# Kernel optimization log

Hardware: AMD Instinct MI355X
Metric: run time of the kernel (lower is better)

Reference implementation:

```python
import jax, jax.numpy as jnp
import numpy as np

WIDTH = 256
HEAD = 16
SCALE = 2
G = WIDTH // HEAD          # 16 groups
NH = G * SCALE             # 32 kernelized heads
EPS = 1e-5
N_NODES = 20000
B_GRAPHS = 1024


def setup_inputs() -> dict:
    key = jax.random.key(0)
    ks = jax.random.split(key, 10)
    x = jax.random.normal(ks[0], (N_NODES, WIDTH), jnp.float32)
    x_res = jax.random.normal(ks[1], (B_GRAPHS, NH, HEAD, HEAD), jnp.float32)
    batch = jnp.sort(jax.random.randint(ks[2], (N_NODES,), 0, B_GRAPHS)).astype(jnp.int64)
    w_pre = jax.random.normal(ks[3], (WIDTH, WIDTH), jnp.float32) * 0.02
    b_pre = jnp.zeros((WIDTH,), jnp.float32)
    # grouped 1x1 convs: [groups, width_scale, head_out, head_in]
    wq = jax.random.normal(ks[4], (G, SCALE, HEAD, HEAD), jnp.float32) * 0.02
    wk = jax.random.normal(ks[5], (G, SCALE, HEAD, HEAD), jnp.float32) * 0.02
    wv = jax.random.normal(ks[6], (G, SCALE, HEAD, HEAD), jnp.float32) * 0.02
    w_post = jax.random.normal(ks[7], (WIDTH, WIDTH * SCALE), jnp.float32) * 0.02
    b_post = jnp.zeros((WIDTH,), jnp.float32)
    log_scale = jnp.full((WIDTH,), np.log(0.01), jnp.float32)
    return {"x": x, "x_res": x_res, "batch": batch, "batch_size": B_GRAPHS,
            "w_pre": w_pre, "b_pre": b_pre, "wq": wq, "wk": wk, "wv": wv,
            "w_post": w_post, "b_post": b_post, "log_scale": log_scale}


def reference(x, x_res, batch, batch_size, w_pre, b_pre, wq, wk, wv, w_post, b_post, log_scale):
    n = x.shape[0]
    # pre: 1x1 conv (= linear) + GroupNorm(affine=False); L=1 so normalize over
    # each group's width_head channels.
    y = x @ w_pre.T + b_pre                       # [N, width]
    yg = y.reshape(n, G, HEAD)                    # [N, G, Hd]
    mu = yg.mean(-1, keepdims=True)
    var = yg.var(-1, keepdims=True)               # biased, as in GroupNorm
    yn = (yg - mu) / jnp.sqrt(var + EPS)          # [N, G, Hd]

    inv_sqrt_h = 1.0 / np.sqrt(HEAD)
    # grouped convs -> kernelized q,k (exp) and v
    xq = jnp.exp(jnp.einsum('ngi,gsoi->ngso', yn, wq) * inv_sqrt_h).reshape(n, NH, HEAD)
    xk = jnp.exp(jnp.einsum('ngi,gsoi->ngso', yn, wk) * inv_sqrt_h).reshape(n, NH, HEAD)
    xv = jnp.einsum('ngi,gsoi->ngso', yn, wv).reshape(n, NH, HEAD)

    # outer product k (x) v then scatter-sum over graphs  [B, NH, Hd, Hd]
    kv = jnp.einsum('bnh,bnv->bnhv', xk, xv)
    kv_sum = jax.ops.segment_sum(kv, batch, num_segments=batch_size) + x_res
    x_res_out = kv_sum

    # per-graph key sum, gathered back to nodes
    k_sum = jax.ops.segment_sum(xk, batch, num_segments=batch_size)[batch]  # [N, NH, Hd]
    denom = jnp.einsum('bnh,bnh->bn', xq, k_sum)                            # [N, NH]
    qn = xq / denom[:, :, None]

    out = jnp.einsum('bnh,bnhv->bnv', qn, kv_sum[batch]).reshape(n, WIDTH * SCALE)
    out = jnp.exp(log_scale) * (out @ w_post.T + b_post)                    # [N, width]
    return (out, x_res_out)
```

## Files before the change

kernel.cpp:

```cpp
#include <hip/hip_runtime.h>
#include <stdint.h>

typedef unsigned int u32;
typedef unsigned short u16;
typedef __attribute__((ext_vector_type(8))) short v8s;
typedef __attribute__((ext_vector_type(4))) float v4f;

#define GN_EPS 1e-5f

__device__ __forceinline__ float bflo(u32 u){ return __uint_as_float(u << 16); }
__device__ __forceinline__ float bfhi(u32 u){ return __uint_as_float(u & 0xffff0000u); }
__device__ __forceinline__ u16 f2bf(float f){
  u32 x = __float_as_uint(f);
  u32 r = (x + 0x7fffu + ((x >> 16) & 1u)) >> 16;
  return (u16)r;
}
__device__ __forceinline__ u32 pack2(float a, float b){
  return (u32)f2bf(a) | ((u32)f2bf(b) << 16);
}
__device__ __forceinline__ void unpack8(const uint4 u, float* f){
  f[0]=bflo(u.x); f[1]=bfhi(u.x); f[2]=bflo(u.y); f[3]=bfhi(u.y);
  f[4]=bflo(u.z); f[5]=bfhi(u.z); f[6]=bflo(u.w); f[7]=bfhi(u.w);
}
__device__ __forceinline__ uint4 loadpack8(const float* __restrict__ p){
  float4 a = *(const float4*)p, b = *(const float4*)(p + 4);
  return make_uint4(pack2(a.x,a.y),pack2(a.z,a.w),pack2(b.x,b.y),pack2(b.z,b.w));
}

__device__ __forceinline__ int getb(const int* __restrict__ b, int is64, int i){
  return b[is64 ? 2*i : i];
}

__global__ __launch_bounds__(256) void k_detect(
    const int* __restrict__ batch, int n, int* __restrict__ flags)
{
  int i = blockIdx.x*256 + threadIdx.x;
  int bad = 0;
  if (i < n - 1 && batch[i] > batch[i + 1]) bad = 1;
  if (__builtin_amdgcn_ballot_w64(bad) != 0 && (threadIdx.x & 63) == 0)
    atomicOr(&flags[0], 1);
}

__global__ __launch_bounds__(256) void k_bounds(
    const int* __restrict__ batch, const int* __restrict__ flags,
    int N, int B, int* __restrict__ bounds)
{
  int i = blockIdx.x*256 + threadIdx.x;
  if (i >= N) return;
  const int is64 = flags[0];
  int b = getb(batch, is64, i);
  int prev = (i == 0) ? -1 : getb(batch, is64, i - 1);
  for (int g = prev + 1; g <= b; g++) bounds[g] = i;
  if (i == N - 1)
    for (int g = b + 1; g <= B; g++) bounds[g] = N;
}

__global__ __launch_bounds__(256) void k_pre(
    const float* __restrict__ x, const float* __restrict__ wpre,
    const float* __restrict__ bpre, float* __restrict__ y, int N, int nbm)
{
  __shared__ __align__(16) u16 As[64*40];
  __shared__ __align__(16) u16 Bs[64*40];
  const int t = threadIdx.x;
  const int bm = blockIdx.x % nbm;
  const int bn = blockIdx.x / nbm;
  const int m_base = bm*64, n_base = bn*64;
  const int w = t >> 6, lane = t & 63;
  const int wm = (w >> 1)*32, wn = (w & 1)*32;
  const int fr = lane & 15, fk = lane >> 4;
  const int srow = t >> 2, scol = (t & 3)*8;

  v4f acc[2][2];
#pragma unroll
  for (int i = 0; i < 2; i++)
#pragma unroll
    for (int j = 0; j < 2; j++) acc[i][j] = (v4f){0.f,0.f,0.f,0.f};

  for (int k0 = 0; k0 < 256; k0 += 32) {
    __syncthreads();
    {
      int gm = m_base + srow;
      uint4 av = make_uint4(0u,0u,0u,0u);
      if (gm < N) av = loadpack8(x + (size_t)gm*256 + k0 + scol);
      *(uint4*)&As[srow*40 + scol] = av;
      uint4 bv = loadpack8(wpre + (size_t)(n_base + srow)*256 + k0 + scol);
      *(uint4*)&Bs[srow*40 + scol] = bv;
    }
    __syncthreads();
    v8s a0 = *(const v8s*)&As[(wm      + fr)*40 + fk*8];
    v8s a1 = *(const v8s*)&As[(wm + 16 + fr)*40 + fk*8];
    v8s b0 = *(const v8s*)&Bs[(wn      + fr)*40 + fk*8];
    v8s b1 = *(const v8s*)&Bs[(wn + 16 + fr)*40 + fk*8];
    acc[0][0] = __builtin_amdgcn_mfma_f32_16x16x32_bf16(a0,b0,acc[0][0],0,0,0);
    acc[0][1] = __builtin_amdgcn_mfma_f32_16x16x32_bf16(a0,b1,acc[0][1],0,0,0);
    acc[1][0] = __builtin_amdgcn_mfma_f32_16x16x32_bf16(a1,b0,acc[1][0],0,0,0);
    acc[1][1] = __builtin_amdgcn_mfma_f32_16x16x32_bf16(a1,b1,acc[1][1],0,0,0);
  }
#pragma unroll
  for (int nj = 0; nj < 2; nj++) {
    int col = n_base + wn + nj*16 + fr;
    float bpv = bpre[col];
#pragma unroll
    for (int mi = 0; mi < 2; mi++) {
#pragma unroll
      for (int r = 0; r < 4; r++) {
        int row = m_base + wm + mi*16 + fk*4 + r;
        if (row < N) y[(size_t)row*256 + col] = acc[mi][nj][r] + bpv;
      }
    }
  }
}

__global__ __launch_bounds__(256) void k_gnqkv(
    const float* __restrict__ y, const float* __restrict__ wq,
    const float* __restrict__ wk, const float* __restrict__ wv,
    u16* __restrict__ qo, u16* __restrict__ ko, u16* __restrict__ vo, int N)
{
  __shared__ __align__(16) float wL[3*512];
  const int t = threadIdx.x;
  const int g = blockIdx.x & 15;
  const int c = blockIdx.x >> 4;
  {
    const float* srcs[3] = {wq, wk, wv};
#pragma unroll
    for (int tz = 0; tz < 3; tz++) {
      wL[tz*512 + t]       = srcs[tz][g*512 + t];
      wL[tz*512 + t + 256] = srcs[tz][g*512 + t + 256];
    }
  }
  __syncthreads();
  const int node = c*256 + t;
  if (node >= N) return;

  const float* yp = y + (size_t)node*256 + g*16;
  float4 v0 = *(const float4*)yp;
  float4 v1 = *(const float4*)(yp + 4);
  float4 v2 = *(const float4*)(yp + 8);
  float4 v3 = *(const float4*)(yp + 12);
  float a[16] = {v0.x,v0.y,v0.z,v0.w, v1.x,v1.y,v1.z,v1.w,
                 v2.x,v2.y,v2.z,v2.w, v3.x,v3.y,v3.z,v3.w};
  float mu = 0.f;
#pragma unroll
  for (int i = 0; i < 16; i++) mu += a[i];
  mu *= 0.0625f;
  float s2 = 0.f;
#pragma unroll
  for (int i = 0; i < 16; i++) { float d = a[i]-mu; s2 = fmaf(d,d,s2); }
  float inv = rsqrtf(s2*0.0625f + GN_EPS);
  float yn[16];
#pragma unroll
  for (int i = 0; i < 16; i++) yn[i] = (a[i]-mu)*inv;

  u16* outs[3] = {qo, ko, vo};
#pragma unroll
  for (int tz = 0; tz < 3; tz++) {
#pragma unroll
    for (int s = 0; s < 2; s++) {
      u32 p[8];
#pragma unroll
      for (int o = 0; o < 16; o++) {
        const float* row = &wL[tz*512 + (s*16 + o)*16];
        float4 W0 = *(const float4*)row;
        float4 W1 = *(const float4*)(row + 4);
        float4 W2 = *(const float4*)(row + 8);
        float4 W3 = *(const float4*)(row + 12);
        float w[16] = {W0.x,W0.y,W0.z,W0.w,W1.x,W1.y,W1.z,W1.w,
                       W2.x,W2.y,W2.z,W2.w,W3.x,W3.y,W3.z,W3.w};
        float d = 0.f;
#pragma unroll
        for (int i = 0; i < 16; i++) d = fmaf(yn[i], w[i], d);
        if (tz < 2) d = __expf(d*0.25f);
        if (o & 1) p[o>>1] |= (u32)f2bf(d) << 16;
        else       p[o>>1]  = (u32)f2bf(d);
      }
      u16* dst = outs[tz] + (size_t)node*512 + g*32 + s*16;
      *(uint4*)dst       = make_uint4(p[0],p[1],p[2],p[3]);
      *(uint4*)(dst + 8) = make_uint4(p[4],p[5],p[6],p[7]);
    }
  }
}

__global__ __launch_bounds__(256) void k_segatt(
    const u16* __restrict__ xk, const u16* __restrict__ xv,
    const u16* __restrict__ xq, const float* __restrict__ xres,
    const int* __restrict__ bounds,
    float* __restrict__ out1, u16* __restrict__ att, int N)
{
  __shared__ __align__(16) float red[2*2592];
  __shared__ float ksred[2*130];
  __shared__ __align__(16) u16 kvsL[8*280];
  __shared__ float kssL[8*17];
  const int t = threadIdx.x;
  const int b  = blockIdx.x >> 2;
  const int H0 = (blockIdx.x & 3) * 8;
  const int lo = bounds[b], hi = bounds[b+1];
  const int ns = t >> 6, nh = (t >> 3) & 7, hp = t & 7;

  float kv[2][16];
#pragma unroll
  for (int r = 0; r < 2; r++)
#pragma unroll
    for (int v = 0; v < 16; v++) kv[r][v] = 0.f;
  float ks0 = 0.f, ks1 = 0.f;

  const size_t koff = (size_t)(H0 + nh)*16 + 2*hp;
  const size_t voff = (size_t)(H0 + nh)*16;
  int node = lo + ns;
  u32 kw = 0; uint4 V0 = make_uint4(0,0,0,0), V1 = make_uint4(0,0,0,0);
  if (node < hi) {
    kw = *(const u32*) (xk + (size_t)node*512 + koff);
    V0 = *(const uint4*)(xv + (size_t)node*512 + voff);
    V1 = *(const uint4*)(xv + (size_t)node*512 + voff + 8);
  }
  while (node < hi) {
    int nxt = node + 4;
    u32 kwn = 0; uint4 V0n = make_uint4(0,0,0,0), V1n = make_uint4(0,0,0,0);
    if (nxt < hi) {
      kwn = *(const u32*) (xk + (size_t)nxt*512 + koff);
      V0n = *(const uint4*)(xv + (size_t)nxt*512 + voff);
      V1n = *(const uint4*)(xv + (size_t)nxt*512 + voff + 8);
    }
    float k0 = bflo(kw), k1 = bfhi(kw);
    float vf[16]; unpack8(V0, vf); unpack8(V1, vf + 8);
    ks0 += k0; ks1 += k1;
#pragma unroll
    for (int v = 0; v < 16; v++) {
      kv[0][v] = fmaf(k0, vf[v], kv[0][v]);
      kv[1][v] = fmaf(k1, vf[v], kv[1][v]);
    }
    kw = kwn; V0 = V0n; V1 = V1n; node = nxt;
  }

  if (ns >= 2) {
    float* s = &red[(ns - 2)*2592];
#pragma unroll
    for (int r = 0; r < 2; r++) {
      float* rp = &s[nh*324 + (2*hp + r)*20];
      *(float4*)rp       = make_float4(kv[r][0], kv[r][1], kv[r][2], kv[r][3]);
      *(float4*)(rp + 4) = make_float4(kv[r][4], kv[r][5], kv[r][6], kv[r][7]);
      *(float4*)(rp + 8) = make_float4(kv[r][8], kv[r][9], kv[r][10],kv[r][11]);
      *(float4*)(rp + 12)= make_float4(kv[r][12],kv[r][13],kv[r][14],kv[r][15]);
    }
    ksred[(ns-2)*130 + nh*16 + 2*hp]     = ks0;
    ksred[(ns-2)*130 + nh*16 + 2*hp + 1] = ks1;
  }
  __syncthreads();
  if (ns < 2) {
    const float* s = &red[ns*2592];
#pragma unroll
    for (int r = 0; r < 2; r++) {
      const float* rp = &s[nh*324 + (2*hp + r)*20];
      float4 R0 = *(const float4*)rp;
      float4 R1 = *(const float4*)(rp + 4);
      float4 R2 = *(const float4*)(rp + 8);
      float4 R3 = *(const float4*)(rp + 12);
      kv[r][0] += R0.x; kv[r][1] += R0.y; kv[r][2] += R0.z; kv[r][3] += R0.w;
      kv[r][4] += R1.x; kv[r][5] += R1.y; kv[r][6] += R1.z; kv[r][7] += R1.w;
      kv[r][8] += R2.x; kv[r][9] += R2.y; kv[r][10]+= R2.z; kv[r][11]+= R2.w;
      kv[r][12]+= R3.x; kv[r][13]+= R3.y; kv[r][14]+= R3.z; kv[r][15]+= R3.w;
    }
    ks0 += ksred[ns*130 + nh*16 + 2*hp];
    ks1 += ksred[ns*130 + nh*16 + 2*hp + 1];
  }
  __syncthreads();
  if (ns == 1) {
#pragma unroll
    for (int r = 0; r < 2; r++) {
      float* rp = &red[nh*324 + (2*hp + r)*20];
      *(float4*)rp       = make_float4(kv[r][0], kv[r][1], kv[r][2], kv[r][3]);
      *(float4*)(rp + 4) = make_float4(kv[r][4], kv[r][5], kv[r][6], kv[r][7]);
      *(float4*)(rp + 8) = make_float4(kv[r][8], kv[r][9], kv[r][10],kv[r][11]);
      *(float4*)(rp + 12)= make_float4(kv[r][12],kv[r][13],kv[r][14],kv[r][15]);
    }
    ksred[nh*16 + 2*hp]     = ks0;
    ksred[nh*16 + 2*hp + 1] = ks1;
  }
  __syncthreads();
  if (ns == 0) {
#pragma unroll
    for (int r = 0; r < 2; r++) {
      const float* rp = &red[nh*324 + (2*hp + r)*20];
      float4 R0 = *(const float4*)rp;
      float4 R1 = *(const float4*)(rp + 4);
      float4 R2 = *(const float4*)(rp + 8);
      float4 R3 = *(const float4*)(rp + 12);
      kv[r][0] += R0.x; kv[r][1] += R0.y; kv[r][2] += R0.z; kv[r][3] += R0.w;
      kv[r][4] += R1.x; kv[r][5] += R1.y; kv[r][6] += R1.z; kv[r][7] += R1.w;
      kv[r][8] += R2.x; kv[r][9] += R2.y; kv[r][10]+= R2.z; kv[r][11]+= R2.w;
      kv[r][12]+= R3.x; kv[r][13]+= R3.y; kv[r][14]+= R3.z; kv[r][15]+= R3.w;
    }
    ks0 += ksred[nh*16 + 2*hp];
    ks1 += ksred[nh*16 + 2*hp + 1];
    kssL[nh*17 + 2*hp]     = ks0;
    kssL[nh*17 + 2*hp + 1] = ks1;

#pragma unroll
    for (int r = 0; r < 2; r++) {
      int h = 2*hp + r;
      size_t idx = ((size_t)(b*32 + H0 + nh)*16 + h)*16;
      const float* xp = xres + idx;
      float4 X0 = *(const float4*)xp;
      float4 X1 = *(const float4*)(xp + 4);
      float4 X2 = *(const float4*)(xp + 8);
      float4 X3 = *(const float4*)(xp + 12);
      float xf[16] = {X0.x,X0.y,X0.z,X0.w,X1.x,X1.y,X1.z,X1.w,
                      X2.x,X2.y,X2.z,X2.w,X3.x,X3.y,X3.z,X3.w};
      float o[16];
#pragma unroll
      for (int j = 0; j < 16; j++) o[j] = kv[r][j] + xf[j];
      float* op = out1 + idx;
      *(float4*)op        = make_float4(o[0],o[1],o[2],o[3]);
      *(float4*)(op + 4)  = make_float4(o[4],o[5],o[6],o[7]);
      *(float4*)(op + 8)  = make_float4(o[8],o[9],o[10],o[11]);
      *(float4*)(op + 12) = make_float4(o[12],o[13],o[14],o[15]);
      u16* lp = &kvsL[nh*280 + h*16];
      *(uint4*)lp       = make_uint4(pack2(o[0],o[1]),  pack2(o[2],o[3]),
                                     pack2(o[4],o[5]),  pack2(o[6],o[7]));
      *(uint4*)(lp + 8) = make_uint4(pack2(o[8],o[9]),  pack2(o[10],o[11]),
                                     pack2(o[12],o[13]),pack2(o[14],o[15]));
    }
  }
  __syncthreads();

  const int nh2 = t & 7, ns2 = t >> 3;
  for (int n0 = lo; n0 < hi; n0 += 32) {
    int nodei = n0 + ns2;
    if (nodei >= hi) continue;
    const u16* qp = xq + (size_t)nodei*512 + (H0 + nh2)*16;
    uint4 Q0 = *(const uint4*)qp;
    uint4 Q1 = *(const uint4*)(qp + 8);
    float q[16]; unpack8(Q0, q); unpack8(Q1, q + 8);
    const float* ksp = &kssL[nh2*17];
    float denom = 0.f;
#pragma unroll
    for (int i = 0; i < 16; i++) denom = fmaf(q[i], ksp[i], denom);
    float inv = 1.0f / fmaxf(denom, 1e-20f);
    float a[16];
#pragma unroll
    for (int v = 0; v < 16; v++) a[v] = 0.f;
    const u16* kvp = &kvsL[nh2*280];
#pragma unroll
    for (int h = 0; h < 16; h++) {
      float qh = q[h] * inv;
      uint4 W0 = *(const uint4*)(kvp + h*16);
      uint4 W1 = *(const uint4*)(kvp + h*16 + 8);
      float w[16]; unpack8(W0, w); unpack8(W1, w + 8);
#pragma unroll
      for (int v = 0; v < 16; v++) a[v] = fmaf(qh, w[v], a[v]);
    }
    u32 p[8];
#pragma unroll
    for (int j = 0; j < 8; j++) p[j] = pack2(a[2*j], a[2*j+1]);
    u16* dst = att + (size_t)nodei*512 + (H0 + nh2)*16;
    *(uint4*)dst       = make_uint4(p[0],p[1],p[2],p[3]);
    *(uint4*)(dst + 8) = make_uint4(p[4],p[5],p[6],p[7]);
  }
}

__global__ __launch_bounds__(256) void k_post(
    const u16* __restrict__ att, const float* __restrict__ wpost,
    const float* __restrict__ bpost, const float* __restrict__ ls,
    float* __restrict__ out0, int N, int nbm)
{
  __shared__ __align__(16) u16 As[64*40];
  __shared__ __align__(16) u16 Bs[64*40];
  const int t = threadIdx.x;
  const int bm = blockIdx.x % nbm;
  const int bn = blockIdx.x / nbm;
  const int m_base = bm*64, n_base = bn*64;
  const int w = t >> 6, lane = t & 63;
  const int wm = (w >> 1)*32, wn = (w & 1)*32;
  const int fr = lane & 15, fk = lane >> 4;
  const int srow = t >> 2, scol = (t & 3)*8;

  v4f acc[2][2];
#pragma unroll
  for (int i = 0; i < 2; i++)
#pragma unroll
    for (int j = 0; j < 2; j++) acc[i][j] = (v4f){0.f,0.f,0.f,0.f};

  for (int k0 = 0; k0 < 512; k0 += 32) {
    __syncthreads();
    {
      int gm = m_base + srow;
      uint4 av = make_uint4(0u,0u,0u,0u);
      if (gm < N) av = *(const uint4*)(att + (size_t)gm*512 + k0 + scol);
      *(uint4*)&As[srow*40 + scol] = av;
      uint4 bv = loadpack8(wpost + (size_t)(n_base + srow)*512 + k0 + scol);
      *(uint4*)&Bs[srow*40 + scol] = bv;
    }
    __syncthreads();
    v8s a0 = *(const v8s*)&As[(wm      + fr)*40 + fk*8];
    v8s a1 = *(const v8s*)&As[(wm + 16 + fr)*40 + fk*8];
    v8s b0 = *(const v8s*)&Bs[(wn      + fr)*40 + fk*8];
    v8s b1 = *(const v8s*)&Bs[(wn + 16 + fr)*40 + fk*8];
    acc[0][0] = __builtin_amdgcn_mfma_f32_16x16x32_bf16(a0,b0,acc[0][0],0,0,0);
    acc[0][1] = __builtin_amdgcn_mfma_f32_16x16x32_bf16(a0,b1,acc[0][1],0,0,0);
    acc[1][0] = __builtin_amdgcn_mfma_f32_16x16x32_bf16(a1,b0,acc[1][0],0,0,0);
    acc[1][1] = __builtin_amdgcn_mfma_f32_16x16x32_bf16(a1,b1,acc[1][1],0,0,0);
  }
#pragma unroll
  for (int nj = 0; nj < 2; nj++) {
    int col = n_base + wn + nj*16 + fr;
    float bpv = bpost[col];
    float e   = __expf(ls[col]);
#pragma unroll
    for (int mi = 0; mi < 2; mi++) {
#pragma unroll
      for (int r = 0; r < 4; r++) {
        int row = m_base + wm + mi*16 + fk*4 + r;
        if (row < N) out0[(size_t)row*256 + col] = e*(acc[mi][nj][r] + bpv);
      }
    }
  }
}

extern "C" void kernel_launch(void* const* d_in, const int* in_sizes, int n_in,
                              void* d_out, int out_size, void* d_ws, size_t ws_size,
                              hipStream_t stream)
{
  const float* x     = (const float*)d_in[0];
  const float* xres  = (const float*)d_in[1];
  const int*   batch = (const int*)d_in[2];
  const float* wpre  = (const float*)d_in[4];
  const float* bpre  = (const float*)d_in[5];
  const float* wq    = (const float*)d_in[6];
  const float* wk    = (const float*)d_in[7];
  const float* wv    = (const float*)d_in[8];
  const float* wpost = (const float*)d_in[9];
  const float* bpost = (const float*)d_in[10];
  const float* ls    = (const float*)d_in[11];

  const int N = in_sizes[0] / 256;
  const int B = in_sizes[1] / 8192;
  const int nbm = (N + 63) / 64;
  const int nchunk = (N + 255) / 256;

  char* ws = (char*)d_ws;
  size_t off = 0;
  int*   flags  = (int*)(ws + off); off += 256;
  int*   bounds = (int*)(ws + off); off += ((size_t)B + 64) * 4;
  float* y      = (float*)(ws + off);
  u16*   att    = (u16*)(ws + off);  off += (size_t)N * 1024;
  u16*   q      = (u16*)(ws + off);  off += (size_t)N * 1024;
  u16*   kten   = (u16*)(ws + off);  off += (size_t)N * 1024;
  u16*   vten   = (u16*)(ws + off);  off += (size_t)N * 1024;

  float* out0 = (float*)d_out;
  float* out1 = out0 + (size_t)N * 256;

  hipMemsetAsync(flags, 0, 4, stream);
  k_detect<<<nchunk,         256, 0, stream>>>(batch, N, flags);
  k_bounds<<<nchunk,         256, 0, stream>>>(batch, flags, N, B, bounds);
  k_pre   <<<nbm * 4,        256, 0, stream>>>(x, wpre, bpre, y, N, nbm);
  k_gnqkv <<<nchunk * 16,    256, 0, stream>>>(y, wq, wk, wv, q, kten, vten, N);
  k_segatt<<<B * 4,          256, 0, stream>>>(kten, vten, q, xres, bounds,
                                               out1, att, N);
  k_post  <<<nbm * 4,        256, 0, stream>>>(att, wpost, bpost, ls, out0, N, nbm);
}
```

Baseline: 136.4 us.

## Split segment attention into per-graph KV reduction and per-node apply kernels

After: 164.9 us. +20.9%, slower.

```diff
diff --git a/kernel.cpp b/kernel.cpp
--- a/kernel.cpp
+++ b/kernel.cpp
@@ -180,16 +180,14 @@
   }
 }
 
-__global__ __launch_bounds__(256) void k_segatt(
+__global__ __launch_bounds__(256) void k_segkv(
     const u16* __restrict__ xk, const u16* __restrict__ xv,
-    const u16* __restrict__ xq, const float* __restrict__ xres,
-    const int* __restrict__ bounds,
-    float* __restrict__ out1, u16* __restrict__ att, int N)
+    const float* __restrict__ xres, const int* __restrict__ bounds,
+    float* __restrict__ out1, u16* __restrict__ kvp,
+    float* __restrict__ kssg, int N)
 {
   __shared__ __align__(16) float red[2*2592];
   __shared__ float ksred[2*130];
-  __shared__ __align__(16) u16 kvsL[8*280];
-  __shared__ float kssL[8*17];
   const int t = threadIdx.x;
   const int b  = blockIdx.x >> 2;
   const int H0 = (blockIdx.x & 3) * 8;
@@ -291,13 +289,13 @@
     }
     ks0 += ksred[nh*16 + 2*hp];
     ks1 += ksred[nh*16 + 2*hp + 1];
-    kssL[nh*17 + 2*hp]     = ks0;
-    kssL[nh*17 + 2*hp + 1] = ks1;
+    const int head = H0 + nh;
+    *(float2*)&kssg[(size_t)b*512 + head*16 + 2*hp] = make_float2(ks0, ks1);
 
 #pragma unroll
     for (int r = 0; r < 2; r++) {
       int h = 2*hp + r;
-      size_t idx = ((size_t)(b*32 + H0 + nh)*16 + h)*16;
+      size_t idx = ((size_t)(b*32 + head)*16 + h)*16;
       const float* xp = xres + idx;
       float4 X0 = *(const float4*)xp;
       float4 X1 = *(const float4*)(xp + 4);
@@ -313,48 +311,63 @@
       *(float4*)(op + 4)  = make_float4(o[4],o[5],o[6],o[7]);
       *(float4*)(op + 8)  = make_float4(o[8],o[9],o[10],o[11]);
       *(float4*)(op + 12) = make_float4(o[12],o[13],o[14],o[15]);
-      u16* lp = &kvsL[nh*280 + h*16];
-      *(uint4*)lp       = make_uint4(pack2(o[0],o[1]),  pack2(o[2],o[3]),
+      u16* kp = kvp + idx;
+      *(uint4*)kp       = make_uint4(pack2(o[0],o[1]),  pack2(o[2],o[3]),
                                      pack2(o[4],o[5]),  pack2(o[6],o[7]));
-      *(uint4*)(lp + 8) = make_uint4(pack2(o[8],o[9]),  pack2(o[10],o[11]),
+      *(uint4*)(kp + 8) = make_uint4(pack2(o[8],o[9]),  pack2(o[10],o[11]),
                                      pack2(o[12],o[13]),pack2(o[14],o[15]));
     }
   }
-  __syncthreads();
-
-  const int nh2 = t & 7, ns2 = t >> 3;
-  for (int n0 = lo; n0 < hi; n0 += 32) {
-    int nodei = n0 + ns2;
-    if (nodei >= hi) continue;
-    const u16* qp = xq + (size_t)nodei*512 + (H0 + nh2)*16;
-    uint4 Q0 = *(const uint4*)qp;
-    uint4 Q1 = *(const uint4*)(qp + 8);
-    float q[16]; unpack8(Q0, q); unpack8(Q1, q + 8);
-    const float* ksp = &kssL[nh2*17];
-    float denom = 0.f;
-#pragma unroll
-    for (int i = 0; i < 16; i++) denom = fmaf(q[i], ksp[i], denom);
-    float inv = 1.0f / fmaxf(denom, 1e-20f);
-    float a[16];
-#pragma unroll
-    for (int v = 0; v < 16; v++) a[v] = 0.f;
-    const u16* kvp = &kvsL[nh2*280];
-#pragma unroll
-    for (int h = 0; h < 16; h++) {
-      float qh = q[h] * inv;
-      uint4 W0 = *(const uint4*)(kvp + h*16);
-      uint4 W1 = *(const uint4*)(kvp + h*16 + 8);
-      float w[16]; unpack8(W0, w); unpack8(W1, w + 8);
-#pragma unroll
-      for (int v = 0; v < 16; v++) a[v] = fmaf(qh, w[v], a[v]);
-    }
-    u32 p[8];
-#pragma unroll
-    for (int j = 0; j < 8; j++) p[j] = pack2(a[2*j], a[2*j+1]);
-    u16* dst = att + (size_t)nodei*512 + (H0 + nh2)*16;
-    *(uint4*)dst       = make_uint4(p[0],p[1],p[2],p[3]);
-    *(uint4*)(dst + 8) = make_uint4(p[4],p[5],p[6],p[7]);
-  }
+}
+
+__global__ __launch_bounds__(256) void k_att2(
+    const u16* __restrict__ xq, const float* __restrict__ kssg,
+    const u16* __restrict__ kvp, const int* __restrict__ batch,
+    const int* __restrict__ flags, u16* __restrict__ att, int N, int B)
+{
+  const int t = threadIdx.x;
+  const int node = blockIdx.x*8 + (t >> 5);
+  const int nh = t & 31;
+  if (node >= N) return;
+  int b = getb(batch, flags[0], node);
+  b = b < 0 ? 0 : (b >= B ? B - 1 : b);
+
+  const u16* qp = xq + (size_t)node*512 + nh*16;
+  uint4 Q0 = *(const uint4*)qp;
+  uint4 Q1 = *(const uint4*)(qp + 8);
+  float q[16]; unpack8(Q0, q); unpack8(Q1, q + 8);
+
+  const float* ksp = kssg + (size_t)b*512 + nh*16;
+  float4 S0 = *(const float4*)ksp;
+  float4 S1 = *(const float4*)(ksp + 4);
+  float4 S2 = *(const float4*)(ksp + 8);
+  float4 S3 = *(const float4*)(ksp + 12);
+  float ks[16] = {S0.x,S0.y,S0.z,S0.w,S1.x,S1.y,S1.z,S1.w,
+                  S2.x,S2.y,S2.z,S2.w,S3.x,S3.y,S3.z,S3.w};
+  float denom = 0.f;
+#pragma unroll
+  for (int i = 0; i < 16; i++) denom = fmaf(q[i], ks[i], denom);
+  float inv = 1.0f / fmaxf(denom, 1e-20f);
+
+  float a[16];
+#pragma unroll
+  for (int v = 0; v < 16; v++) a[v] = 0.f;
+  const u16* kvr = kvp + (size_t)(b*32 + nh)*256;
+#pragma unroll
+  for (int h = 0; h < 16; h++) {
+    float qh = q[h] * inv;
+    uint4 W0 = *(const uint4*)(kvr + h*16);
+    uint4 W1 = *(const uint4*)(kvr + h*16 + 8);
+    float w[16]; unpack8(W0, w); unpack8(W1, w + 8);
+#pragma unroll
+    for (int v = 0; v < 16; v++) a[v] = fmaf(qh, w[v], a[v]);
+  }
+  u32 p[8];
+#pragma unroll
+  for (int j = 0; j < 8; j++) p[j] = pack2(a[2*j], a[2*j+1]);
+  u16* dst = att + (size_t)node*512 + nh*16;
+  *(uint4*)dst       = make_uint4(p[0],p[1],p[2],p[3]);
+  *(uint4*)(dst + 8) = make_uint4(p[4],p[5],p[6],p[7]);
 }
 
 __global__ __launch_bounds__(256) void k_post(
@@ -445,6 +458,8 @@
   u16*   q      = (u16*)(ws + off);  off += (size_t)N * 1024;
   u16*   kten   = (u16*)(ws + off);  off += (size_t)N * 1024;
   u16*   vten   = (u16*)(ws + off);  off += (size_t)N * 1024;
+  u16*   kvp    = (u16*)(ws + off);  off += (size_t)B * 16384;
+  float* kssg   = (float*)(ws + off); off += (size_t)B * 2048;
 
   float* out0 = (float*)d_out;
   float* out1 = out0 + (size_t)N * 256;
@@ -454,7 +469,9 @@
   k_bounds<<<nchunk,         256, 0, stream>>>(batch, flags, N, B, bounds);
   k_pre   <<<nbm * 4,        256, 0, stream>>>(x, wpre, bpre, y, N, nbm);
   k_gnqkv <<<nchunk * 16,    256, 0, stream>>>(y, wq, wk, wv, q, kten, vten, N);
-  k_segatt<<<B * 4,          256, 0, stream>>>(kten, vten, q, xres, bounds,
-                                               out1, att, N);
+  k_segkv <<<B * 4,          256, 0, stream>>>(kten, vten, xres, bounds,
+                                               out1, kvp, kssg, N);
+  k_att2  <<<(N + 7) / 8,    256, 0, stream>>>(q, kssg, kvp, batch, flags,
+                                               att, N, B);
   k_post  <<<nbm * 4,        256, 0, stream>>>(att, wpost, bpost, ls, out0, N, nbm);
 }
```
